# Kernel tuning notes

Measured on AMD Instinct MI355X. Metric: run time of the kernel, lower is better.

Reference implementation:

```python
import jax, jax.numpy as jnp
import numpy as np

N_NODES = 20000
N_EDGES = 320000
N_GRAPHS = 32
C = 256
L = 4
IN_DIM = 739
EDGE_DIM = 2 * C + 6
LN_EPS = 1e-5


def _layernorm(x, g, b):
    mu = jnp.mean(x, axis=-1, keepdims=True)
    var = jnp.mean(jnp.square(x - mu), axis=-1, keepdims=True)
    return (x - mu) * jax.lax.rsqrt(var + LN_EPS) * g + b


def setup_inputs() -> dict:
    key = jax.random.key(0)
    ks = jax.random.split(key, 20)
    d = {}
    d["x"] = jax.random.normal(ks[0], (N_NODES, IN_DIM), jnp.float32)
    d["x_pos"] = jax.random.normal(ks[1], (N_NODES, 3), jnp.float32)
    d["edge_index"] = jax.random.randint(ks[2], (2, N_EDGES), 0, N_NODES, jnp.int32)
    d["batch"] = jnp.sort(jax.random.randint(ks[3], (N_NODES,), 0, N_GRAPHS, jnp.int32))
    s = 0.02
    d["dense_w"] = jax.random.normal(ks[4], (IN_DIM, C), jnp.float32) * s
    d["dense_b"] = jnp.zeros((C,), jnp.float32)
    d["d1_w"] = jax.random.normal(ks[5], (L, C, C), jnp.float32) * s
    d["d1_b"] = jnp.zeros((L, C), jnp.float32)
    d["ln1_g"] = jnp.ones((L, EDGE_DIM), jnp.float32)
    d["ln1_b"] = jnp.zeros((L, EDGE_DIM), jnp.float32)
    d["w1_w"] = jax.random.normal(ks[6], (L, EDGE_DIM, 4), jnp.float32) * s
    d["w1_b"] = jnp.zeros((L, 4), jnp.float32)
    d["ln2_g"] = jnp.ones((L, 4), jnp.float32)
    d["ln2_b"] = jnp.zeros((L, 4), jnp.float32)
    d["w2_w"] = jax.random.normal(ks[7], (L, 4, 1), jnp.float32) * s
    d["w2_b"] = jnp.zeros((L, 1), jnp.float32)
    d["d2_w"] = jax.random.normal(ks[8], (L, C, C), jnp.float32) * s
    d["d2_b"] = jnp.zeros((L, C), jnp.float32)
    d["head_w"] = jax.random.normal(ks[9], (C, 1), jnp.float32) * s
    d["head_b"] = jnp.zeros((1,), jnp.float32)
    return d


def reference(x, x_pos, edge_index, batch, dense_w, dense_b, d1_w, d1_b,
              ln1_g, ln1_b, w1_w, w1_b, ln2_g, ln2_b, w2_w, w2_b,
              d2_w, d2_b, head_w, head_b):
    n = x.shape[0]
    src, dst = edge_index[0], edge_index[1]
    h = x @ dense_w + dense_b  # [N, C]
    for l in range(d1_w.shape[0]):
        # message: dense1 -> GELU (dropout is identity in eval)
        m = jax.nn.gelu(h @ d1_w[l] + d1_b[l], approximate=False)  # [N, C]
        sx = m[src]                                                # [E, C]
        # edge-MLP input: [src_x, dst_x, src_pos, dst_pos]
        e = jnp.concatenate([sx, m[dst], x_pos[src], x_pos[dst]], axis=-1)  # [E, 2C+6]
        e = _layernorm(e, ln1_g[l], ln1_b[l])
        e = jax.nn.gelu(e @ w1_w[l] + w1_b[l], approximate=False)  # [E, 4]
        e = _layernorm(e, ln2_g[l], ln2_b[l])
        w = jax.nn.sigmoid(e @ w2_w[l] + w2_b[l])                  # [E, 1]
        agg = jax.ops.segment_sum(sx * w, dst, num_segments=n)     # [N, C]
        # update: dense2 -> GELU
        h = jax.nn.gelu(agg @ d2_w[l] + d2_b[l], approximate=False)
    # global mean pool over graphs
    sums = jax.ops.segment_sum(h, batch, num_segments=N_GRAPHS)           # [G, C]
    cnts = jax.ops.segment_sum(jnp.ones((n, 1), h.dtype), batch, num_segments=N_GRAPHS)
    pooled = sums / jnp.maximum(cnts, 1.0)
    return pooled @ head_w + head_b  # [G, 1]
```

## Files before the change

kernel.cpp:

```cpp
#include <hip/hip_runtime.h>
#include <math.h>

#define N_NODES 20000
#define N_EDGES 320000
#define N_GRAPHS 32
#define CDIM 256
#define IN_DIMV 739
#define KPAD_DENSE 768
#define ED_DIM 518
#define NLAYERS 4
#define LN_EPS 1e-5f
#define SCAN_BLOCKS ((N_NODES + 255) / 256)

typedef _Float16 f16x8 __attribute__((ext_vector_type(8)));
typedef _Float16 f16x4 __attribute__((ext_vector_type(4)));
typedef float f32x4 __attribute__((ext_vector_type(4)));

__device__ __forceinline__ float gelu_exact(float x) {
    return 0.5f * x * (1.f + erff(x * 0.7071067811865475f));
}

__global__ __launch_bounds__(256)
void prep_all(const float* __restrict__ ln1_g, const float* __restrict__ ln1_b,
              const float* __restrict__ w1_w, float* __restrict__ cw,
              float* __restrict__ SgSb,
              const float* __restrict__ x, _Float16* __restrict__ xh,
              const float* __restrict__ dense_w, _Float16* __restrict__ wt_dense,
              const float* __restrict__ d1_w, const float* __restrict__ d2_w,
              _Float16* __restrict__ wt_sq, int* __restrict__ deg) {
    __shared__ float smem[2048 + 64];
    int b = blockIdx.x, tid = threadIdx.x;
    if (b < 79) {
        int i = b * 256 + tid;
        if (i < N_NODES) deg[i] = 0;
    } else if (b < 83) {
        int l = b - 79;
        float sg[4] = {0, 0, 0, 0}, sb[4] = {0, 0, 0, 0};
        for (int i = tid; i < ED_DIM; i += 256) {
            float g = ln1_g[l * ED_DIM + i];
            float bb = ln1_b[l * ED_DIM + i];
            float4 w = *(const float4*)&w1_w[(size_t)(l * ED_DIM + i) * 4];
            float4 c = make_float4(g * w.x, g * w.y, g * w.z, g * w.w);
            *(float4*)&cw[(size_t)(l * ED_DIM + i) * 4] = c;
            sg[0] += c.x; sg[1] += c.y; sg[2] += c.z; sg[3] += c.w;
            sb[0] += bb * w.x; sb[1] += bb * w.y; sb[2] += bb * w.z; sb[3] += bb * w.w;
        }
        for (int c = 0; c < 4; c++) { smem[tid * 8 + c] = sg[c]; smem[tid * 8 + 4 + c] = sb[c]; }
        __syncthreads();
        for (int s = 128; s > 0; s >>= 1) {
            if (tid < s)
                for (int c = 0; c < 8; c++) smem[tid * 8 + c] += smem[(tid + s) * 8 + c];
            __syncthreads();
        }
        if (tid < 8) SgSb[l * 8 + tid] = smem[tid];
    } else if (b < 275) {
        int q = b - 83;
        int kt = q >> 3, nt = q & 7;
        int i = tid >> 5, j = tid & 31;
        float* T = smem;
#pragma unroll
        for (int ii = 0; ii < 4; ii++) {
            int k = kt * 32 + i + ii * 8;
            T[(i + ii * 8) * 33 + j] = (k < IN_DIMV) ? dense_w[(size_t)k * 256 + nt * 32 + j] : 0.f;
        }
        __syncthreads();
#pragma unroll
        for (int ii = 0; ii < 4; ii++) {
            int n = nt * 32 + i + ii * 8;
            wt_dense[(size_t)n * KPAD_DENSE + kt * 32 + j] = (_Float16)T[j * 33 + i + ii * 8];
        }
    } else if (b < 787) {
        int q = b - 275;
        int z = q >> 6, kt = (q >> 3) & 7, nt = q & 7;
        const float* W = (z < 4) ? d1_w + (size_t)z * 65536 : d2_w + (size_t)(z - 4) * 65536;
        _Float16* O = wt_sq + (size_t)z * 65536;
        int i = tid >> 5, j = tid & 31;
        float* T = smem;
#pragma unroll
        for (int ii = 0; ii < 4; ii++)
            T[(i + ii * 8) * 33 + j] = W[(size_t)(kt * 32 + i + ii * 8) * 256 + nt * 32 + j];
        __syncthreads();
#pragma unroll
        for (int ii = 0; ii < 4; ii++)
            O[(size_t)(nt * 32 + i + ii * 8) * 256 + kt * 32 + j] = (_Float16)T[j * 33 + i + ii * 8];
    } else {
        const int TOT = N_NODES * KPAD_DENSE;
        const int STRIDE = 2048 * 256;
        for (int idx = (b - 787) * 256 + tid; idx < TOT; idx += STRIDE) {
            int n = idx / KPAD_DENSE, k = idx - n * KPAD_DENSE;
            xh[idx] = (k < IN_DIMV) ? (_Float16)x[(size_t)n * IN_DIMV + k] : (_Float16)0.f;
        }
    }
}

__global__ void hist_gstart_kernel(const int* __restrict__ ei, const int* __restrict__ batch,
                                   int* __restrict__ deg, int* __restrict__ gstart) {
    int e = blockIdx.x * 256 + threadIdx.x;
    if (e < N_EDGES) atomicAdd(&deg[ei[N_EDGES + e]], 1);
    if (e < N_NODES) {
        int b = batch[e];
        int bprev = (e == 0) ? -1 : batch[e - 1];
        for (int g = bprev + 1; g <= b; g++) gstart[g] = e;
        if (e == N_NODES - 1)
            for (int g = b + 1; g <= N_GRAPHS; g++) gstart[g] = N_NODES;
    }
}

__global__ __launch_bounds__(256)
void scan1_kernel(const int* __restrict__ deg, int* __restrict__ bsum) {
    __shared__ int red[256];
    int t = threadIdx.x;
    int i = blockIdx.x * 256 + t;
    red[t] = (i < N_NODES) ? deg[i] : 0;
    __syncthreads();
    for (int s = 128; s > 0; s >>= 1) {
        if (t < s) red[t] += red[t + s];
        __syncthreads();
    }
    if (t == 0) bsum[blockIdx.x] = red[0];
}

__global__ __launch_bounds__(128)
void scan2_kernel(const int* __restrict__ bsum, int* __restrict__ boff) {
    __shared__ int s[128];
    int t = threadIdx.x;
    int v = (t < SCAN_BLOCKS) ? bsum[t] : 0;
    s[t] = v;
    __syncthreads();
    for (int off = 1; off < 128; off <<= 1) {
        int o = (t >= off) ? s[t - off] : 0;
        __syncthreads();
        s[t] += o;
        __syncthreads();
    }
    if (t < SCAN_BLOCKS) boff[t] = s[t] - v;
}

__global__ __launch_bounds__(256)
void scan3_kernel(const int* __restrict__ deg, const int* __restrict__ boff,
                  int* __restrict__ row_start, int* __restrict__ cursor) {
    __shared__ int s[256];
    int t = threadIdx.x;
    int i = blockIdx.x * 256 + t;
    int v = (i < N_NODES) ? deg[i] : 0;
    s[t] = v;
    __syncthreads();
    for (int off = 1; off < 256; off <<= 1) {
        int o = (t >= off) ? s[t - off] : 0;
        __syncthreads();
        s[t] += o;
        __syncthreads();
    }
    int base = boff[blockIdx.x];
    int excl = base + s[t] - v;
    if (i < N_NODES) {
        row_start[i] = excl;
        cursor[i] = excl;
    }
    if (i == N_NODES - 1) row_start[N_NODES] = base + s[t];
}

__global__ void scatter_kernel(const int* __restrict__ ei, int* __restrict__ cursor,
                               int* __restrict__ csr_src, int* __restrict__ slot) {
    int e = blockIdx.x * 256 + threadIdx.x;
    if (e < N_EDGES) {
        int d = ei[N_EDGES + e];
        int pos = atomicAdd(&cursor[d], 1);
        csr_src[pos] = ei[e];
        slot[e] = pos;
    }
}

template <bool GELU>
__global__ __launch_bounds__(256)
void gemm_mfma(const _Float16* __restrict__ A, const _Float16* __restrict__ Bt,
               const float* __restrict__ bias, _Float16* __restrict__ C,
               int Kpad) {
    __shared__ __align__(16) _Float16 As[32 * 72];
    __shared__ __align__(16) _Float16 Bs[128 * 72];
    int tid = threadIdx.x;
    int row0 = blockIdx.x * 32;
    int col0 = blockIdx.y * 128;
    int wave = tid >> 6, lane = tid & 63;
    int quad = lane >> 4, lrow = lane & 15;
    int wrow = wave >> 1, wcol = wave & 1;

    int ar = tid >> 3, ak8 = (tid & 7) * 8;
    int br = tid >> 1, bh = (tid & 1) * 32;

    const _Float16* Arow = &A[(size_t)(row0 + ar) * Kpad];
    const _Float16* Brow = &Bt[(size_t)(col0 + br) * Kpad];

    int ntiles = Kpad >> 6;
    uint4 a_raw = *(const uint4*)&Arow[ak8];
    uint4 b_raw0 = *(const uint4*)&Brow[bh];
    uint4 b_raw1 = *(const uint4*)&Brow[bh + 8];
    uint4 b_raw2 = *(const uint4*)&Brow[bh + 16];
    uint4 b_raw3 = *(const uint4*)&Brow[bh + 24];

    f32x4 acc[4];
#pragma unroll
    for (int t = 0; t < 4; t++) acc[t] = (f32x4){0.f, 0.f, 0.f, 0.f};

    for (int kt = 0; kt < ntiles; ++kt) {
        *(uint4*)&As[ar * 72 + ak8] = a_raw;
        *(uint4*)&Bs[br * 72 + bh] = b_raw0;
        *(uint4*)&Bs[br * 72 + bh + 8] = b_raw1;
        *(uint4*)&Bs[br * 72 + bh + 16] = b_raw2;
        *(uint4*)&Bs[br * 72 + bh + 24] = b_raw3;
        __syncthreads();

        if (kt + 1 < ntiles) {
            int k0 = (kt + 1) << 6;
            a_raw = *(const uint4*)&Arow[k0 + ak8];
            b_raw0 = *(const uint4*)&Brow[k0 + bh];
            b_raw1 = *(const uint4*)&Brow[k0 + bh + 8];
            b_raw2 = *(const uint4*)&Brow[k0 + bh + 16];
            b_raw3 = *(const uint4*)&Brow[k0 + bh + 24];
        }

#pragma unroll
        for (int h = 0; h < 2; h++) {
            f16x8 af = *(const f16x8*)&As[(wrow * 16 + lrow) * 72 + h * 32 + quad * 8];
#pragma unroll
            for (int t = 0; t < 4; t++) {
                f16x8 bf = *(const f16x8*)&Bs[((wcol * 4 + t) * 16 + lrow) * 72 + h * 32 + quad * 8];
                acc[t] = __builtin_amdgcn_mfma_f32_16x16x32_f16(af, bf, acc[t], 0, 0, 0);
            }
        }
        __syncthreads();
    }

    int orow = row0 + wrow * 16 + quad * 4;
#pragma unroll
    for (int t = 0; t < 4; t++) {
        int col = col0 + (wcol * 4 + t) * 16 + lrow;
        float bv = bias[col];
#pragma unroll
        for (int r = 0; r < 4; r++) {
            float v = acc[t][r] + bv;
            C[(size_t)(orow + r) * 256 + col] = (_Float16)(GELU ? gelu_exact(v) : v);
        }
    }
}

__global__ __launch_bounds__(256)
void node_summary_kernel(const _Float16* __restrict__ m, const float* __restrict__ cw,
                         float* __restrict__ ns) {
    __shared__ __align__(16) float4 s_cw[512];
    int tid = threadIdx.x;
    for (int i = tid; i < 512; i += 256) s_cw[i] = *(const float4*)&cw[(size_t)i * 4];
    __syncthreads();
    int n = blockIdx.x * 4 + (tid >> 6);
    if (n >= N_NODES) return;
    int lane = tid & 63;
    f16x4 a4 = *(const f16x4*)&m[(size_t)n * CDIM + lane * 4];
    float av[4] = {(float)a4[0], (float)a4[1], (float)a4[2], (float)a4[3]};
    float Q1 = 0.f, Q2 = 0.f, P1[4] = {0, 0, 0, 0}, P2[4] = {0, 0, 0, 0};
#pragma unroll
    for (int j = 0; j < 4; j++) {
        Q1 += av[j];
        Q2 += av[j] * av[j];
        float4 c0 = s_cw[lane * 4 + j];
        float4 c1 = s_cw[256 + lane * 4 + j];
        P1[0] += av[j] * c0.x; P1[1] += av[j] * c0.y; P1[2] += av[j] * c0.z; P1[3] += av[j] * c0.w;
        P2[0] += av[j] * c1.x; P2[1] += av[j] * c1.y; P2[2] += av[j] * c1.z; P2[3] += av[j] * c1.w;
    }
#pragma unroll
    for (int off = 1; off < 64; off <<= 1) {
        Q1 += __shfl_xor(Q1, off, 64);
        Q2 += __shfl_xor(Q2, off, 64);
        P1[0] += __shfl_xor(P1[0], off, 64);
        P1[1] += __shfl_xor(P1[1], off, 64);
        P1[2] += __shfl_xor(P1[2], off, 64);
        P1[3] += __shfl_xor(P1[3], off, 64);
        P2[0] += __shfl_xor(P2[0], off, 64);
        P2[1] += __shfl_xor(P2[1], off, 64);
        P2[2] += __shfl_xor(P2[2], off, 64);
        P2[3] += __shfl_xor(P2[3], off, 64);
    }
    if (lane == 0) {
        float* p = &ns[(size_t)n * 12];
        *(float4*)p = make_float4(P1[0], P1[1], P1[2], P1[3]);
        *(float4*)(p + 4) = make_float4(P2[0], P2[1], P2[2], P2[3]);
        p[8] = Q1;
        p[9] = Q2;
    }
}

__global__ __launch_bounds__(256)
void edge_weight_kernel(const float* __restrict__ ns, const float* __restrict__ x_pos,
                        const int* __restrict__ ei, const float* __restrict__ cw,
                        const float* __restrict__ SgSb, const float* __restrict__ w1_b,
                        const float* __restrict__ ln2_g, const float* __restrict__ ln2_b,
                        const float* __restrict__ w2_w, const float* __restrict__ w2_b,
                        const int* __restrict__ slot, float* __restrict__ w_csr) {
    int e = blockIdx.x * 256 + threadIdx.x;
    if (e >= N_EDGES) return;
    int s = ei[e], d = ei[N_EDGES + e];
    const float* nss = &ns[(size_t)s * 12];
    const float* nsd = &ns[(size_t)d * 12];
    float4 p1 = *(const float4*)nss;
    float4 p2 = *(const float4*)(nsd + 4);
    float S1 = nss[8] + nsd[8];
    float S2 = nss[9] + nsd[9];
    float D[4] = {p1.x + p2.x, p1.y + p2.y, p1.z + p2.z, p1.w + p2.w};
    float ps[6];
    ps[0] = x_pos[(size_t)s * 3 + 0];
    ps[1] = x_pos[(size_t)s * 3 + 1];
    ps[2] = x_pos[(size_t)s * 3 + 2];
    ps[3] = x_pos[(size_t)d * 3 + 0];
    ps[4] = x_pos[(size_t)d * 3 + 1];
    ps[5] = x_pos[(size_t)d * 3 + 2];
#pragma unroll
    for (int k = 0; k < 6; k++) {
        S1 += ps[k];
        S2 += ps[k] * ps[k];
        float4 c = *(const float4*)&cw[(size_t)(512 + k) * 4];
        D[0] += ps[k] * c.x; D[1] += ps[k] * c.y; D[2] += ps[k] * c.z; D[3] += ps[k] * c.w;
    }
    const float inv = 1.f / 518.f;
    float mu = S1 * inv;
    float var = fmaf(-mu, mu, S2 * inv);
    float rstd = rsqrtf(var + LN_EPS);
    float t[4];
#pragma unroll
    for (int c = 0; c < 4; c++)
        t[c] = gelu_exact(rstd * (D[c] - mu * SgSb[c]) + SgSb[4 + c] + w1_b[c]);
    float mu2 = 0.25f * (t[0] + t[1] + t[2] + t[3]);
    float var2 = 0.25f * ((t[0] - mu2) * (t[0] - mu2) + (t[1] - mu2) * (t[1] - mu2) +
                          (t[2] - mu2) * (t[2] - mu2) + (t[3] - mu2) * (t[3] - mu2));
    float r2 = rsqrtf(var2 + LN_EPS);
    float z = w2_b[0];
#pragma unroll
    for (int c = 0; c < 4; c++)
        z += ((t[c] - mu2) * r2 * ln2_g[c] + ln2_b[c]) * w2_w[c];
    w_csr[slot[e]] = 1.f / (1.f + expf(-z));
}

__global__ __launch_bounds__(256)
void agg_kernel(const _Float16* __restrict__ m, const int* __restrict__ csr_src,
                const float* __restrict__ w_csr, const int* __restrict__ row_start,
                _Float16* __restrict__ agg) {
    int n = blockIdx.x * 4 + (threadIdx.x >> 6);
    if (n >= N_NODES) return;
    int lane = threadIdx.x & 63;
    int beg = row_start[n], end = row_start[n + 1];
    float a0 = 0.f, a1 = 0.f, a2 = 0.f, a3 = 0.f;
    int j = beg;
    for (; j + 8 <= end; j += 8) {
        int si[8];
        float wi[8];
#pragma unroll
        for (int u = 0; u < 8; u++) { si[u] = csr_src[j + u]; wi[u] = w_csr[j + u]; }
        f16x4 v[8];
#pragma unroll
        for (int u = 0; u < 8; u++) v[u] = *(const f16x4*)&m[(size_t)si[u] * CDIM + lane * 4];
#pragma unroll
        for (int u = 0; u < 8; u++) {
            a0 = fmaf(wi[u], (float)v[u][0], a0);
            a1 = fmaf(wi[u], (float)v[u][1], a1);
            a2 = fmaf(wi[u], (float)v[u][2], a2);
            a3 = fmaf(wi[u], (float)v[u][3], a3);
        }
    }
    for (; j < end; j++) {
        int s = csr_src[j];
        float w = w_csr[j];
        f16x4 v = *(const f16x4*)&m[(size_t)s * CDIM + lane * 4];
        a0 = fmaf(w, (float)v[0], a0);
        a1 = fmaf(w, (float)v[1], a1);
        a2 = fmaf(w, (float)v[2], a2);
        a3 = fmaf(w, (float)v[3], a3);
    }
    f16x4 o;
    o[0] = (_Float16)a0; o[1] = (_Float16)a1; o[2] = (_Float16)a2; o[3] = (_Float16)a3;
    *(f16x4*)&agg[(size_t)n * CDIM + lane * 4] = o;
}

__global__ __launch_bounds__(256)
void node_dot_kernel(const _Float16* __restrict__ h, const float* __restrict__ head_w,
                     float* __restrict__ sdot) {
    int n = blockIdx.x * 4 + (threadIdx.x >> 6);
    if (n >= N_NODES) return;
    int lane = threadIdx.x & 63;
    f16x4 v = *(const f16x4*)&h[(size_t)n * CDIM + lane * 4];
    float4 w = *(const float4*)&head_w[lane * 4];
    float p = (float)v[0] * w.x + (float)v[1] * w.y + (float)v[2] * w.z + (float)v[3] * w.w;
#pragma unroll
    for (int off = 1; off < 64; off <<= 1) p += __shfl_xor(p, off, 64);
    if (lane == 0) sdot[n] = p;
}

__global__ __launch_bounds__(256)
void final_head_kernel(const float* __restrict__ sdot, const int* __restrict__ gstart,
                       const float* __restrict__ head_b, float* __restrict__ out) {
    int g = blockIdx.x;
    int t = threadIdx.x;
    int beg = gstart[g], end = gstart[g + 1];
    float s = 0.f;
    for (int i = beg + t; i < end; i += 256) s += sdot[i];
    __shared__ float red[256];
    red[t] = s;
    __syncthreads();
    for (int k = 128; k > 0; k >>= 1) {
        if (t < k) red[t] += red[t + k];
        __syncthreads();
    }
    if (t == 0) out[g] = red[0] / fmaxf((float)(end - beg), 1.f) + head_b[0];
}

extern "C" void kernel_launch(void* const* d_in, const int* in_sizes, int n_in,
                              void* d_out, int out_size, void* d_ws, size_t ws_size,
                              hipStream_t stream) {
    const float* x       = (const float*)d_in[0];
    const float* x_pos   = (const float*)d_in[1];
    const int*   ei      = (const int*)d_in[2];
    const int*   batch   = (const int*)d_in[3];
    const float* dense_w = (const float*)d_in[4];
    const float* dense_b = (const float*)d_in[5];
    const float* d1_w    = (const float*)d_in[6];
    const float* d1_b    = (const float*)d_in[7];
    const float* ln1_g   = (const float*)d_in[8];
    const float* ln1_b   = (const float*)d_in[9];
    const float* w1_w    = (const float*)d_in[10];
    const float* w1_b    = (const float*)d_in[11];
    const float* ln2_g   = (const float*)d_in[12];
    const float* ln2_b   = (const float*)d_in[13];
    const float* w2_w    = (const float*)d_in[14];
    const float* w2_b    = (const float*)d_in[15];
    const float* d2_w    = (const float*)d_in[16];
    const float* d2_b    = (const float*)d_in[17];
    const float* head_w  = (const float*)d_in[18];
    const float* head_b  = (const float*)d_in[19];
    float* out = (float*)d_out;

    _Float16* hbuf0 = (_Float16*)d_ws;
    _Float16* hbuf1 = hbuf0 + (size_t)N_NODES * CDIM;
    _Float16* xh    = hbuf1 + (size_t)N_NODES * CDIM;
    _Float16* wt_dense = xh + (size_t)N_NODES * KPAD_DENSE;
    _Float16* wt_sq    = wt_dense + (size_t)256 * KPAD_DENSE;
    float* cw    = (float*)(wt_sq + (size_t)8 * 256 * 256);
    float* SgSb  = cw + (size_t)NLAYERS * ED_DIM * 4;
    float* ns    = SgSb + NLAYERS * 8;
    float* sdot  = ns + (size_t)N_NODES * 12;
    float* w_csr = sdot + N_NODES;
    int* gstart    = (int*)(w_csr + N_EDGES);
    int* deg       = gstart + N_GRAPHS + 1;
    int* row_start = deg + N_NODES;
    int* cursor    = row_start + N_NODES + 1;
    int* csr_src   = cursor + N_NODES;
    int* slot      = csr_src + N_EDGES;
    int* bsum      = slot + N_EDGES;
    int* boff      = bsum + SCAN_BLOCKS;

    prep_all<<<2835, 256, 0, stream>>>(ln1_g, ln1_b, w1_w, cw, SgSb,
                                       x, xh, dense_w, wt_dense, d1_w, d2_w, wt_sq, deg);

    hist_gstart_kernel<<<(N_EDGES + 255) / 256, 256, 0, stream>>>(ei, batch, deg, gstart);
    scan1_kernel<<<SCAN_BLOCKS, 256, 0, stream>>>(deg, bsum);
    scan2_kernel<<<1, 128, 0, stream>>>(bsum, boff);
    scan3_kernel<<<SCAN_BLOCKS, 256, 0, stream>>>(deg, boff, row_start, cursor);
    scatter_kernel<<<(N_EDGES + 255) / 256, 256, 0, stream>>>(ei, cursor, csr_src, slot);

    const dim3 GGRID(N_NODES / 32, 2);
    gemm_mfma<false><<<GGRID, 256, 0, stream>>>(xh, wt_dense, dense_b, hbuf0, KPAD_DENSE);

    _Float16* h = hbuf0;
    _Float16* other = hbuf1;
    for (int l = 0; l < NLAYERS; l++) {
        gemm_mfma<true><<<GGRID, 256, 0, stream>>>(
            h, wt_sq + (size_t)l * 65536, d1_b + l * CDIM, other, CDIM);
        node_summary_kernel<<<(N_NODES + 3) / 4, 256, 0, stream>>>(
            other, cw + (size_t)l * ED_DIM * 4, ns);
        edge_weight_kernel<<<(N_EDGES + 255) / 256, 256, 0, stream>>>(
            ns, x_pos, ei, cw + (size_t)l * ED_DIM * 4, SgSb + l * 8, w1_b + l * 4,
            ln2_g + l * 4, ln2_b + l * 4, w2_w + l * 4, w2_b + l, slot, w_csr);
        agg_kernel<<<(N_NODES + 3) / 4, 256, 0, stream>>>(other, csr_src, w_csr, row_start, h);
        gemm_mfma<true><<<GGRID, 256, 0, stream>>>(
            h, wt_sq + (size_t)(4 + l) * 65536, d2_b + l * CDIM, other, CDIM);
        _Float16* tmp = h; h = other; other = tmp;
    }

    node_dot_kernel<<<(N_NODES + 3) / 4, 256, 0, stream>>>(h, head_w, sdot);
    final_head_kernel<<<N_GRAPHS, 256, 0, stream>>>(sdot, gstart, head_b, out);
}
```

Before: 538.5 us.

## Fuse fp32-to-fp16 input conversion into dense GEMM and head dot into last GEMM

Result: no change. 529.3 us (-1.7%).

```diff
diff --git a/kernel.cpp b/kernel.cpp
--- a/kernel.cpp
+++ b/kernel.cpp
@@ -24,10 +24,10 @@
 void prep_all(const float* __restrict__ ln1_g, const float* __restrict__ ln1_b,
               const float* __restrict__ w1_w, float* __restrict__ cw,
               float* __restrict__ SgSb,
-              const float* __restrict__ x, _Float16* __restrict__ xh,
               const float* __restrict__ dense_w, _Float16* __restrict__ wt_dense,
               const float* __restrict__ d1_w, const float* __restrict__ d2_w,
-              _Float16* __restrict__ wt_sq, int* __restrict__ deg) {
+              _Float16* __restrict__ wt_sq, int* __restrict__ deg,
+              float* __restrict__ sdot) {
     __shared__ float smem[2048 + 64];
     int b = blockIdx.x, tid = threadIdx.x;
     if (b < 79) {
@@ -84,12 +84,8 @@
         for (int ii = 0; ii < 4; ii++)
             O[(size_t)(nt * 32 + i + ii * 8) * 256 + kt * 32 + j] = (_Float16)T[j * 33 + i + ii * 8];
     } else {
-        const int TOT = N_NODES * KPAD_DENSE;
-        const int STRIDE = 2048 * 256;
-        for (int idx = (b - 787) * 256 + tid; idx < TOT; idx += STRIDE) {
-            int n = idx / KPAD_DENSE, k = idx - n * KPAD_DENSE;
-            xh[idx] = (k < IN_DIMV) ? (_Float16)x[(size_t)n * IN_DIMV + k] : (_Float16)0.f;
-        }
+        int i = (b - 787) * 256 + tid;
+        if (i < N_NODES) sdot[i] = 0.f;
     }
 }
 
@@ -171,11 +167,9 @@
     }
 }
 
-template <bool GELU>
-__global__ __launch_bounds__(256)
-void gemm_mfma(const _Float16* __restrict__ A, const _Float16* __restrict__ Bt,
-               const float* __restrict__ bias, _Float16* __restrict__ C,
-               int Kpad) {
+__global__ __launch_bounds__(256)
+void gemm_dense(const float* __restrict__ A, const _Float16* __restrict__ Bt,
+                const float* __restrict__ bias, _Float16* __restrict__ C) {
     __shared__ __align__(16) _Float16 As[32 * 72];
     __shared__ __align__(16) _Float16 Bs[128 * 72];
     int tid = threadIdx.x;
@@ -188,10 +182,93 @@
     int ar = tid >> 3, ak8 = (tid & 7) * 8;
     int br = tid >> 1, bh = (tid & 1) * 32;
 
-    const _Float16* Arow = &A[(size_t)(row0 + ar) * Kpad];
-    const _Float16* Brow = &Bt[(size_t)(col0 + br) * Kpad];
-
-    int ntiles = Kpad >> 6;
+    const float* Arow = &A[(size_t)(row0 + ar) * IN_DIMV];
+    const _Float16* Brow = &Bt[(size_t)(col0 + br) * KPAD_DENSE];
+
+    const int ntiles = KPAD_DENSE >> 6;
+    float a_f[8];
+#pragma unroll
+    for (int j = 0; j < 8; j++) {
+        int gk = ak8 + j;
+        a_f[j] = (gk < IN_DIMV) ? Arow[gk] : 0.f;
+    }
+    uint4 b_raw0 = *(const uint4*)&Brow[bh];
+    uint4 b_raw1 = *(const uint4*)&Brow[bh + 8];
+    uint4 b_raw2 = *(const uint4*)&Brow[bh + 16];
+    uint4 b_raw3 = *(const uint4*)&Brow[bh + 24];
+
+    f32x4 acc[4];
+#pragma unroll
+    for (int t = 0; t < 4; t++) acc[t] = (f32x4){0.f, 0.f, 0.f, 0.f};
+
+    for (int kt = 0; kt < ntiles; ++kt) {
+        f16x8 ah;
+#pragma unroll
+        for (int j = 0; j < 8; j++) ah[j] = (_Float16)a_f[j];
+        *(f16x8*)&As[ar * 72 + ak8] = ah;
+        *(uint4*)&Bs[br * 72 + bh] = b_raw0;
+        *(uint4*)&Bs[br * 72 + bh + 8] = b_raw1;
+        *(uint4*)&Bs[br * 72 + bh + 16] = b_raw2;
+        *(uint4*)&Bs[br * 72 + bh + 24] = b_raw3;
+        __syncthreads();
+
+        if (kt + 1 < ntiles) {
+            int k0 = (kt + 1) << 6;
+#pragma unroll
+            for (int j = 0; j < 8; j++) {
+                int gk = k0 + ak8 + j;
+                a_f[j] = (gk < IN_DIMV) ? Arow[gk] : 0.f;
+            }
+            b_raw0 = *(const uint4*)&Brow[k0 + bh];
+            b_raw1 = *(const uint4*)&Brow[k0 + bh + 8];
+            b_raw2 = *(const uint4*)&Brow[k0 + bh + 16];
+            b_raw3 = *(const uint4*)&Brow[k0 + bh + 24];
+        }
+
+#pragma unroll
+        for (int h = 0; h < 2; h++) {
+            f16x8 af = *(const f16x8*)&As[(wrow * 16 + lrow) * 72 + h * 32 + quad * 8];
+#pragma unroll
+            for (int t = 0; t < 4; t++) {
+                f16x8 bf = *(const f16x8*)&Bs[((wcol * 4 + t) * 16 + lrow) * 72 + h * 32 + quad * 8];
+                acc[t] = __builtin_amdgcn_mfma_f32_16x16x32_f16(af, bf, acc[t], 0, 0, 0);
+            }
+        }
+        __syncthreads();
+    }
+
+    int orow = row0 + wrow * 16 + quad * 4;
+#pragma unroll
+    for (int t = 0; t < 4; t++) {
+        int col = col0 + (wcol * 4 + t) * 16 + lrow;
+        float bv = bias[col];
+#pragma unroll
+        for (int r = 0; r < 4; r++)
+            C[(size_t)(orow + r) * 256 + col] = (_Float16)(acc[t][r] + bv);
+    }
+}
+
+template <bool GELU, bool DOT>
+__global__ __launch_bounds__(256)
+void gemm_mfma(const _Float16* __restrict__ A, const _Float16* __restrict__ Bt,
+               const float* __restrict__ bias, _Float16* __restrict__ C,
+               const float* __restrict__ head_w, float* __restrict__ sdot) {
+    __shared__ __align__(16) _Float16 As[32 * 72];
+    __shared__ __align__(16) _Float16 Bs[128 * 72];
+    int tid = threadIdx.x;
+    int row0 = blockIdx.x * 32;
+    int col0 = blockIdx.y * 128;
+    int wave = tid >> 6, lane = tid & 63;
+    int quad = lane >> 4, lrow = lane & 15;
+    int wrow = wave >> 1, wcol = wave & 1;
+
+    int ar = tid >> 3, ak8 = (tid & 7) * 8;
+    int br = tid >> 1, bh = (tid & 1) * 32;
+
+    const _Float16* Arow = &A[(size_t)(row0 + ar) * CDIM];
+    const _Float16* Brow = &Bt[(size_t)(col0 + br) * CDIM];
+
+    const int ntiles = CDIM >> 6;
     uint4 a_raw = *(const uint4*)&Arow[ak8];
     uint4 b_raw0 = *(const uint4*)&Brow[bh];
     uint4 b_raw1 = *(const uint4*)&Brow[bh + 8];
@@ -232,14 +309,37 @@
     }
 
     int orow = row0 + wrow * 16 + quad * 4;
-#pragma unroll
-    for (int t = 0; t < 4; t++) {
-        int col = col0 + (wcol * 4 + t) * 16 + lrow;
-        float bv = bias[col];
+    if (DOT) {
+        float dp[4] = {0.f, 0.f, 0.f, 0.f};
+#pragma unroll
+        for (int t = 0; t < 4; t++) {
+            int col = col0 + (wcol * 4 + t) * 16 + lrow;
+            float hw = head_w[col];
+            float bv = bias[col];
+#pragma unroll
+            for (int r = 0; r < 4; r++)
+                dp[r] += gelu_exact(acc[t][r] + bv) * hw;
+        }
 #pragma unroll
         for (int r = 0; r < 4; r++) {
-            float v = acc[t][r] + bv;
-            C[(size_t)(orow + r) * 256 + col] = (_Float16)(GELU ? gelu_exact(v) : v);
+#pragma unroll
+            for (int off = 1; off < 16; off <<= 1)
+                dp[r] += __shfl_xor(dp[r], off, 64);
+        }
+        if (lrow == 0) {
+#pragma unroll
+            for (int r = 0; r < 4; r++) atomicAdd(&sdot[orow + r], dp[r]);
+        }
+    } else {
+#pragma unroll
+        for (int t = 0; t < 4; t++) {
+            int col = col0 + (wcol * 4 + t) * 16 + lrow;
+            float bv = bias[col];
+#pragma unroll
+            for (int r = 0; r < 4; r++) {
+                float v = acc[t][r] + bv;
+                C[(size_t)(orow + r) * 256 + col] = (_Float16)(GELU ? gelu_exact(v) : v);
+            }
         }
     }
 }
@@ -376,20 +476,6 @@
     f16x4 o;
     o[0] = (_Float16)a0; o[1] = (_Float16)a1; o[2] = (_Float16)a2; o[3] = (_Float16)a3;
     *(f16x4*)&agg[(size_t)n * CDIM + lane * 4] = o;
-}
-
-__global__ __launch_bounds__(256)
-void node_dot_kernel(const _Float16* __restrict__ h, const float* __restrict__ head_w,
-                     float* __restrict__ sdot) {
-    int n = blockIdx.x * 4 + (threadIdx.x >> 6);
-    if (n >= N_NODES) return;
-    int lane = threadIdx.x & 63;
-    f16x4 v = *(const f16x4*)&h[(size_t)n * CDIM + lane * 4];
-    float4 w = *(const float4*)&head_w[lane * 4];
-    float p = (float)v[0] * w.x + (float)v[1] * w.y + (float)v[2] * w.z + (float)v[3] * w.w;
-#pragma unroll
-    for (int off = 1; off < 64; off <<= 1) p += __shfl_xor(p, off, 64);
-    if (lane == 0) sdot[n] = p;
 }
 
 __global__ __launch_bounds__(256)
@@ -437,8 +523,7 @@
 
     _Float16* hbuf0 = (_Float16*)d_ws;
     _Float16* hbuf1 = hbuf0 + (size_t)N_NODES * CDIM;
-    _Float16* xh    = hbuf1 + (size_t)N_NODES * CDIM;
-    _Float16* wt_dense = xh + (size_t)N_NODES * KPAD_DENSE;
+    _Float16* wt_dense = hbuf1 + (size_t)N_NODES * CDIM;
     _Float16* wt_sq    = wt_dense + (size_t)256 * KPAD_DENSE;
     float* cw    = (float*)(wt_sq + (size_t)8 * 256 * 256);
     float* SgSb  = cw + (size_t)NLAYERS * ED_DIM * 4;
@@ -454,8 +539,8 @@
     int* bsum      = slot + N_EDGES;
     int* boff      = bsum + SCAN_BLOCKS;
 
-    prep_all<<<2835, 256, 0, stream>>>(ln1_g, ln1_b, w1_w, cw, SgSb,
-                                       x, xh, dense_w, wt_dense, d1_w, d2_w, wt_sq, deg);
+    prep_all<<<866, 256, 0, stream>>>(ln1_g, ln1_b, w1_w, cw, SgSb,
+                                      dense_w, wt_dense, d1_w, d2_w, wt_sq, deg, sdot);
 
     hist_gstart_kernel<<<(N_EDGES + 255) / 256, 256, 0, stream>>>(ei, batch, deg, gstart);
     scan1_kernel<<<SCAN_BLOCKS, 256, 0, stream>>>(deg, bsum);
@@ -464,24 +549,28 @@
     scatter_kernel<<<(N_EDGES + 255) / 256, 256, 0, stream>>>(ei, cursor, csr_src, slot);
 
     const dim3 GGRID(N_NODES / 32, 2);
-    gemm_mfma<false><<<GGRID, 256, 0, stream>>>(xh, wt_dense, dense_b, hbuf0, KPAD_DENSE);
+    gemm_dense<<<GGRID, 256, 0, stream>>>(x, wt_dense, dense_b, hbuf0);
 
     _Float16* h = hbuf0;
     _Float16* other = hbuf1;
     for (int l = 0; l < NLAYERS; l++) {
-        gemm_mfma<true><<<GGRID, 256, 0, stream>>>(
-            h, wt_sq + (size_t)l * 65536, d1_b + l * CDIM, other, CDIM);
+        gemm_mfma<true, false><<<GGRID, 256, 0, stream>>>(
+            h, wt_sq + (size_t)l * 65536, d1_b + l * CDIM, other, nullptr, nullptr);
         node_summary_kernel<<<(N_NODES + 3) / 4, 256, 0, stream>>>(
             other, cw + (size_t)l * ED_DIM * 4, ns);
         edge_weight_kernel<<<(N_EDGES + 255) / 256, 256, 0, stream>>>(
             ns, x_pos, ei, cw + (size_t)l * ED_DIM * 4, SgSb + l * 8, w1_b + l * 4,
             ln2_g + l * 4, ln2_b + l * 4, w2_w + l * 4, w2_b + l, slot, w_csr);
         agg_kernel<<<(N_NODES + 3) / 4, 256, 0, stream>>>(other, csr_src, w_csr, row_start, h);
-        gemm_mfma<true><<<GGRID, 256, 0, stream>>>(
-            h, wt_sq + (size_t)(4 + l) * 65536, d2_b + l * CDIM, other, CDIM);
+        if (l < NLAYERS - 1) {
+            gemm_mfma<true, false><<<GGRID, 256, 0, stream>>>(
+                h, wt_sq + (size_t)(4 + l) * 65536, d2_b + l * CDIM, other, nullptr, nullptr);
+        } else {
+            gemm_mfma<true, true><<<GGRID, 256, 0, stream>>>(
+                h, wt_sq + (size_t)(4 + l) * 65536, d2_b + l * CDIM, other, head_w, sdot);
+        }
         _Float16* tmp = h; h = other; other = tmp;
     }
 
-    node_dot_kernel<<<(N_NODES + 3) / 4, 256, 0, stream>>>(h, head_w, sdot);
     final_head_kernel<<<N_GRAPHS, 256, 0, stream>>>(sdot, gstart, head_b, out);
 }
```
